# Performance work log

Hardware: AMD Instinct MI355X
Metric: run time of the kernel (lower is better)

Reference implementation:

```python
import jax, jax.numpy as jnp
import numpy as np

B, S, D, H, DH, DF, L = 8, 785, 128, 8, 64, 512, 6
HW = 28
CIN = 512


def setup_inputs() -> dict:
    key = jax.random.key(0)
    ks = iter(jax.random.split(key, 40))
    n = lambda shape, s=0.02: jax.random.normal(next(ks), shape, dtype=jnp.float32) * s
    inp = {}
    # conv stem (1x1 conv, no bias) + BN (eval mode) params
    inp["conv_w"] = n((D, CIN), 0.05)
    inp["bn_gamma"] = 1.0 + n((D,), 0.05)
    inp["bn_beta"] = n((D,), 0.05)
    inp["bn_mean"] = n((D,), 0.05)
    inp["bn_var"] = 1.0 + 0.1 * jax.random.uniform(next(ks), (D,), dtype=jnp.float32)
    # encoder embeddings
    inp["pos_emb"] = n((1, S, D))
    inp["cls_token"] = n((1, 1, D))
    # per-layer stacked params
    inp["Wq"] = n((L, D, H * DH)); inp["bq"] = jnp.zeros((L, H * DH), jnp.float32)
    inp["Wk"] = n((L, D, H * DH)); inp["bk"] = jnp.zeros((L, H * DH), jnp.float32)
    inp["Wv"] = n((L, D, H * DH)); inp["bv"] = jnp.zeros((L, H * DH), jnp.float32)
    inp["Wo"] = n((L, H * DH, D)); inp["bo"] = jnp.zeros((L, D), jnp.float32)
    inp["ln1_g"] = jnp.ones((L, D), jnp.float32); inp["ln1_b"] = jnp.zeros((L, D), jnp.float32)
    inp["ffn_w1"] = n((L, D, DF)); inp["ffn_b1"] = jnp.zeros((L, DF), jnp.float32)
    inp["ffn_w2"] = n((L, DF, D)); inp["ffn_b2"] = jnp.zeros((L, D), jnp.float32)
    inp["ln2_g"] = jnp.ones((L, D), jnp.float32); inp["ln2_b"] = jnp.zeros((L, D), jnp.float32)
    # MLP head (both Linear layers bias=False)
    inp["proj_w1"] = n((D, 512)); inp["proj_w2"] = n((512, 1))
    # forward tensor args
    inp["enc_inputs"] = jnp.ones((B, S), dtype=jnp.int32)  # no padding -> mask all False
    inp["x"] = jax.random.normal(next(ks), (B, CIN, HW, HW), dtype=jnp.float32)
    inp["y"] = jax.random.normal(next(ks), (B, CIN, HW, HW), dtype=jnp.float32)
    return inp


def _layer_norm(z, g, b, eps=1e-12):
    mu = z.mean(-1, keepdims=True)
    var = ((z - mu) ** 2).mean(-1, keepdims=True)
    return (z - mu) * jax.lax.rsqrt(var + eps) * g + b


def reference(conv_w, bn_gamma, bn_beta, bn_mean, bn_var, pos_emb, cls_token,
              Wq, bq, Wk, bk, Wv, bv, Wo, bo, ln1_g, ln1_b,
              ffn_w1, ffn_b1, ffn_w2, ffn_b2, ln2_g, ln2_b,
              proj_w1, proj_w2, enc_inputs, x, y):
    def conv_enc(z):
        z = jnp.einsum('bchw,dc->bdhw', z, conv_w)  # 1x1 conv, no bias
        inv = jax.lax.rsqrt(bn_var + 1e-5)
        z = (z - bn_mean[None, :, None, None]) * inv[None, :, None, None]
        z = z * bn_gamma[None, :, None, None] + bn_beta[None, :, None, None]
        return jax.nn.relu(z)

    x = conv_enc(x)
    y = conv_enc(y)
    max_val = jnp.maximum(x.max(), y.max())
    x = x / max_val
    y = y / max_val
    b = x.shape[0]
    x = x.reshape(b, D, -1).transpose(0, 2, 1)  # [b, hw, D]
    y = y.reshape(b, D, -1).transpose(0, 2, 1)

    cls = jnp.broadcast_to(cls_token, (b, 1, D))
    xs = jnp.concatenate([cls, x], axis=1) + pos_emb    # evolving stream (K, V)
    xf = jnp.concatenate([cls, y], axis=1) + pos_emb    # fixed stream (Q)

    pad_mask = (enc_inputs == 0)[:, None, None, :]      # [b,1,1,S], broadcast over heads & queries
    scale = 1.0 / jnp.sqrt(jnp.float32(DH))

    for i in range(L):
        q = (xf @ Wq[i] + bq[i]).reshape(b, S, H, DH).transpose(0, 2, 1, 3)
        k = (xs @ Wk[i] + bk[i]).reshape(b, S, H, DH).transpose(0, 2, 1, 3)
        v = (xs @ Wv[i] + bv[i]).reshape(b, S, H, DH).transpose(0, 2, 1, 3)
        scores = jnp.einsum('bhqd,bhkd->bhqk', q, k) * scale
        scores = jnp.where(pad_mask, jnp.float32(-1e9), scores)
        probs = jax.nn.softmax(scores, axis=-1)
        ctx = jnp.einsum('bhqk,bhkd->bhqd', probs, v)
        ctx = ctx.transpose(0, 2, 1, 3).reshape(b, S, H * DH)
        att = ctx @ Wo[i] + bo[i]
        xs = _layer_norm(xs + att, ln1_g[i], ln1_b[i])
        ff = jax.nn.gelu(xs @ ffn_w1[i] + ffn_b1[i], approximate=False) @ ffn_w2[i] + ffn_b2[i]
        xs = _layer_norm(ff + xs, ln2_g[i], ln2_b[i])

    h = jax.nn.relu(xs[:, 0, :] @ proj_w1)
    return h @ proj_w2  # [b, 1]
```

## Files before the change

### kernel.cpp

```cpp
#include <hip/hip_runtime.h>
#include <hip/hip_bf16.h>
#include <math.h>

typedef float f4 __attribute__((ext_vector_type(4)));
typedef _Float16 h8 __attribute__((ext_vector_type(8)));
typedef float f32x4 __attribute__((ext_vector_type(4)));

#define NB 8
#define NS 785
#define ND 128
#define NH 8
#define NDH 64
#define NDF 512
#define NL 6
#define NP 784
#define NCIN 512
#define NM (NB*NS)

__global__ __launch_bounds__(256) void conv_bn_relu_kernel(
    const float* __restrict__ x, const float* __restrict__ w,
    const float* __restrict__ gamma, const float* __restrict__ beta,
    const float* __restrict__ mean, const float* __restrict__ var,
    float* __restrict__ enc, unsigned int* __restrict__ maxv)
{
    __shared__ float xt[64][17];
    __shared__ float wt[64][132];
    __shared__ float red[4];
    const int b  = blockIdx.y;
    const int p0 = blockIdx.x * 16;
    const int t  = threadIdx.x;
    const int pl = (t & 3) * 4;
    const int dl = (t >> 2) * 2;
    float acc[2][4] = {};
    for (int c0 = 0; c0 < NCIN; c0 += 64) {
        __syncthreads();
        {
            int cc = t >> 2, pp = (t & 3) * 4;
            f4 v = *(const f4*)&x[(size_t)(b*NCIN + c0 + cc)*NP + p0 + pp];
            xt[cc][pp+0] = v[0]; xt[cc][pp+1] = v[1]; xt[cc][pp+2] = v[2]; xt[cc][pp+3] = v[3];
        }
        #pragma unroll
        for (int i = 0; i < 8; i++) {
            int e = t + i*256;
            int d = e >> 4, c4 = (e & 15) * 4;
            f4 v = *(const f4*)&w[(size_t)d*NCIN + c0 + c4];
            wt[c4+0][d] = v[0]; wt[c4+1][d] = v[1]; wt[c4+2][d] = v[2]; wt[c4+3][d] = v[3];
        }
        __syncthreads();
        #pragma unroll 8
        for (int cc = 0; cc < 64; cc++) {
            float w0 = wt[cc][dl], w1 = wt[cc][dl+1];
            float x0 = xt[cc][pl+0], x1 = xt[cc][pl+1], x2 = xt[cc][pl+2], x3 = xt[cc][pl+3];
            acc[0][0] += w0*x0; acc[0][1] += w0*x1; acc[0][2] += w0*x2; acc[0][3] += w0*x3;
            acc[1][0] += w1*x0; acc[1][1] += w1*x1; acc[1][2] += w1*x2; acc[1][3] += w1*x3;
        }
    }
    float lmax = 0.f;
    #pragma unroll
    for (int i = 0; i < 2; i++) {
        int d = dl + i;
        float inv = rsqrtf(var[d] + 1e-5f);
        float sc = gamma[d] * inv;
        float sh = beta[d] - mean[d] * sc;
        #pragma unroll
        for (int j = 0; j < 4; j++) {
            float vo = fmaxf(acc[i][j]*sc + sh, 0.f);
            lmax = fmaxf(lmax, vo);
            enc[(size_t)(b*NP + p0 + pl + j)*ND + d] = vo;
        }
    }
    for (int o = 1; o < 64; o <<= 1) lmax = fmaxf(lmax, __shfl_xor(lmax, o));
    if ((t & 63) == 0) red[t >> 6] = lmax;
    __syncthreads();
    if (t == 0) {
        float m2 = fmaxf(fmaxf(red[0], red[1]), fmaxf(red[2], red[3]));
        atomicMax(maxv, __float_as_uint(m2));
    }
}

__global__ __launch_bounds__(256) void wconv_kernel(
    const float* __restrict__ w0, const float* __restrict__ w1,
    const float* __restrict__ w2, const float* __restrict__ w3,
    const float* __restrict__ w4, const float* __restrict__ w5,
    _Float16* o0, _Float16* o1, _Float16* o2,
    _Float16* o3, _Float16* o4, _Float16* o5)
{
    int t = blockIdx.x*256 + threadIdx.x;
    int type = t / 393216, off = t % 393216;
    const float* in; _Float16* outp;
    switch (type) {
        case 0: in = w0; outp = o0; break;
        case 1: in = w1; outp = o1; break;
        case 2: in = w2; outp = o2; break;
        case 3: in = w3; outp = o3; break;
        case 4: in = w4; outp = o4; break;
        default: in = w5; outp = o5; break;
    }
    outp[off] = (_Float16)in[off];
}

__global__ void assemble_kernel(
    const float* __restrict__ encx, const float* __restrict__ ency,
    const float* __restrict__ cls, const float* __restrict__ pos,
    const float* __restrict__ maxv, float* __restrict__ xs,
    _Float16* __restrict__ xsh, _Float16* __restrict__ xfh)
{
    int i = blockIdx.x*256 + threadIdx.x;
    int d = i & 127;
    int s = (i >> 7) % NS;
    int b = i / (NS*ND);
    float inv = 1.f / maxv[0];
    float pv = pos[s*ND + d];
    float xv, yv;
    if (s == 0) { xv = cls[d]; yv = cls[d]; }
    else {
        int idx = (b*NP + s - 1)*ND + d;
        xv = encx[idx]*inv; yv = ency[idx]*inv;
    }
    float sx = xv + pv, fx = yv + pv;
    xs[i]  = sx;
    xsh[i] = (_Float16)sx;
    xfh[i] = (_Float16)fx;
}

template<int ACT, int OUTH>
__global__ __launch_bounds__(256) void mfma_gemm_kernel(
    const _Float16* __restrict__ A, const _Float16* __restrict__ W,
    const float* __restrict__ bias, void* __restrict__ Cv,
    int M, int N, int K)
{
    __shared__ _Float16 At[128][40];
    __shared__ _Float16 Wt[64][40];
    const int bm = blockIdx.x * 128, bn = blockIdx.y * 64;
    const int t = threadIdx.x;
    const int lane = t & 63;
    const int wave = t >> 6;
    const int m0 = (wave >> 1) * 64;
    const int n0 = (wave & 1) * 32;
    const int lrow = lane & 15, lhi = lane >> 4;
    f32x4 acc[4][2] = {};

    for (int k0 = 0; k0 < K; k0 += 32) {
        __syncthreads();
        {
            int r = t >> 1, sg = (t & 1) * 16;
            int row = bm + r;
            h8 lo = {}, hi = {};
            if (row < M) {
                const _Float16* src = &A[(size_t)row*K + k0 + sg];
                lo = *(const h8*)&src[0];
                hi = *(const h8*)&src[8];
            }
            *(h8*)&At[r][sg]     = lo;
            *(h8*)&At[r][sg + 8] = hi;
        }
        {
            int kk = t >> 3, nseg = (t & 7) * 8;
            h8 v = *(const h8*)&W[(size_t)(k0 + kk)*N + bn + nseg];
            #pragma unroll
            for (int i = 0; i < 8; i++) Wt[nseg + i][kk] = v[i];
        }
        __syncthreads();
        h8 af[4], bf[2];
        #pragma unroll
        for (int mf = 0; mf < 4; mf++) af[mf] = *(const h8*)&At[m0 + mf*16 + lrow][lhi*8];
        #pragma unroll
        for (int nf = 0; nf < 2; nf++) bf[nf] = *(const h8*)&Wt[n0 + nf*16 + lrow][lhi*8];
        #pragma unroll
        for (int mf = 0; mf < 4; mf++)
            #pragma unroll
            for (int nf = 0; nf < 2; nf++)
                acc[mf][nf] = __builtin_amdgcn_mfma_f32_16x16x32_f16(af[mf], bf[nf], acc[mf][nf], 0, 0, 0);
    }

    #pragma unroll
    for (int nf = 0; nf < 2; nf++) {
        int col = bn + n0 + nf*16 + lrow;
        float bv = bias[col];
        #pragma unroll
        for (int mf = 0; mf < 4; mf++) {
            #pragma unroll
            for (int r = 0; r < 4; r++) {
                int row = bm + m0 + mf*16 + lhi*4 + r;
                if (row < M) {
                    float v = acc[mf][nf][r] + bv;
                    if (ACT == 1) v = 0.5f * v * (1.f + erff(v * 0.70710678118654752f));
                    if (OUTH) ((_Float16*)Cv)[(size_t)row*N + col] = (_Float16)v;
                    else      ((float*)Cv)[(size_t)row*N + col] = v;
                }
            }
        }
    }
}

__global__ __launch_bounds__(256) void attn_mfma_kernel(
    const _Float16* __restrict__ Q, const _Float16* __restrict__ K,
    const _Float16* __restrict__ V, const int* __restrict__ enc,
    _Float16* __restrict__ O)
{
    __shared__ _Float16 Ks[64][68];
    __shared__ _Float16 Vt[64][68];
    __shared__ _Float16 Ps[4][16][68];
    __shared__ float madd[832];
    const int b = blockIdx.x, h = blockIdx.y, qt = blockIdx.z;
    const int q0 = qt * 64;
    const int t = threadIdx.x, lane = t & 63, w = t >> 6;
    const int lrow = lane & 15, lhi = lane >> 4;

    for (int i = t; i < 832; i += 256)
        madd[i] = (i < NS && enc[b*NS + i] == 0) ? -1e9f : 0.f;

    h8 qf[2] = {};
    {
        int qrow = q0 + w*16 + lrow;
        if (qrow < NS) {
            const _Float16* src = &Q[(size_t)(b*NS + qrow)*512 + h*64];
            #pragma unroll
            for (int ks = 0; ks < 2; ks++)
                qf[ks] = *(const h8*)&src[ks*32 + lhi*8];
        }
    }

    float m[4], l[4];
    f32x4 acc[4] = {};
    #pragma unroll
    for (int r = 0; r < 4; r++) { m[r] = -INFINITY; l[r] = 0.f; }

    for (int kt = 0; kt < 13; kt++) {
        int k0 = kt * 64;
        __syncthreads();
        {
            int r = t >> 2, c0 = (t & 3) * 16;
            int s = k0 + r;
            h8 lo = {}, hi = {};
            if (s < NS) {
                const _Float16* src = &K[(size_t)(b*NS + s)*512 + h*64 + c0];
                lo = *(const h8*)&src[0];
                hi = *(const h8*)&src[8];
            }
            *(h8*)&Ks[r][c0]     = lo;
            *(h8*)&Ks[r][c0 + 8] = hi;
        }
        {
            int r = t >> 2, c0 = (t & 3) * 16;
            int s = k0 + r;
            h8 a = {}, c = {};
            if (s < NS) {
                const _Float16* src = &V[(size_t)(b*NS + s)*512 + h*64 + c0];
                a = *(const h8*)&src[0];
                c = *(const h8*)&src[8];
            }
            #pragma unroll
            for (int i = 0; i < 8; i++) Vt[c0 + i][r] = a[i];
            #pragma unroll
            for (int i = 0; i < 8; i++) Vt[c0 + 8 + i][r] = c[i];
        }
        __syncthreads();

        f32x4 sc[4] = {};
        #pragma unroll
        for (int nf = 0; nf < 4; nf++)
            #pragma unroll
            for (int ks = 0; ks < 2; ks++) {
                h8 bf = *(const h8*)&Ks[nf*16 + lrow][ks*32 + lhi*8];
                sc[nf] = __builtin_amdgcn_mfma_f32_16x16x32_f16(qf[ks], bf, sc[nf], 0, 0, 0);
            }
        #pragma unroll
        for (int nf = 0; nf < 4; nf++) {
            int kk = k0 + nf*16 + lrow;
            float ma = madd[kk];
            bool oob = (kk >= NS);
            #pragma unroll
            for (int r = 0; r < 4; r++) {
                float v = sc[nf][r] * 0.125f + ma;
                sc[nf][r] = oob ? -INFINITY : v;
            }
        }
        float corr[4];
        #pragma unroll
        for (int r = 0; r < 4; r++) {
            float mt = fmaxf(fmaxf(sc[0][r], sc[1][r]), fmaxf(sc[2][r], sc[3][r]));
            mt = fmaxf(mt, __shfl_xor(mt, 1));
            mt = fmaxf(mt, __shfl_xor(mt, 2));
            mt = fmaxf(mt, __shfl_xor(mt, 4));
            mt = fmaxf(mt, __shfl_xor(mt, 8));
            float mn = fmaxf(m[r], mt);
            corr[r] = __expf(m[r] - mn);
            m[r] = mn;
            float ps = 0.f;
            #pragma unroll
            for (int nf = 0; nf < 4; nf++) {
                float p = __expf(sc[nf][r] - mn);
                sc[nf][r] = p;
                ps += p;
            }
            ps += __shfl_xor(ps, 1);
            ps += __shfl_xor(ps, 2);
            ps += __shfl_xor(ps, 4);
            ps += __shfl_xor(ps, 8);
            l[r] = l[r] * corr[r] + ps;
        }
        #pragma unroll
        for (int nf = 0; nf < 4; nf++)
            #pragma unroll
            for (int r = 0; r < 4; r++)
                Ps[w][lhi*4 + r][nf*16 + lrow] = (_Float16)sc[nf][r];
        asm volatile("s_waitcnt lgkmcnt(0)" ::: "memory");
        __builtin_amdgcn_sched_barrier(0);
        #pragma unroll
        for (int nf = 0; nf < 4; nf++)
            #pragma unroll
            for (int r = 0; r < 4; r++) acc[nf][r] *= corr[r];
        #pragma unroll
        for (int nf = 0; nf < 4; nf++)
            #pragma unroll
            for (int ks = 0; ks < 2; ks++) {
                h8 pf = *(const h8*)&Ps[w][lrow][ks*32 + lhi*8];
                h8 vf = *(const h8*)&Vt[nf*16 + lrow][ks*32 + lhi*8];
                acc[nf] = __builtin_amdgcn_mfma_f32_16x16x32_f16(pf, vf, acc[nf], 0, 0, 0);
            }
    }
    #pragma unroll
    for (int nf = 0; nf < 4; nf++)
        #pragma unroll
        for (int r = 0; r < 4; r++) {
            int row = q0 + w*16 + lhi*4 + r;
            if (row < NS)
                O[(size_t)(b*NS + row)*512 + h*64 + nf*16 + lrow] = (_Float16)(acc[nf][r] / l[r]);
        }
}

__global__ __launch_bounds__(256) void res_ln_kernel(
    const float* X, const float* __restrict__ R,
    const float* __restrict__ g, const float* __restrict__ be,
    float* out, _Float16* __restrict__ outh)
{
    int row = blockIdx.x*4 + (threadIdx.x >> 6);
    int lane = threadIdx.x & 63;
    const float* xr = X + (size_t)row*128;
    const float* rr = R + (size_t)row*128;
    float a0 = xr[lane] + rr[lane];
    float a1 = xr[lane+64] + rr[lane+64];
    float s = a0 + a1;
    for (int o = 1; o < 64; o <<= 1) s += __shfl_xor(s, o);
    float mean = s * (1.f/128.f);
    float e0 = a0 - mean, e1 = a1 - mean;
    float vs = e0*e0 + e1*e1;
    for (int o = 1; o < 64; o <<= 1) vs += __shfl_xor(vs, o);
    float rstd = rsqrtf(vs * (1.f/128.f) + 1e-12f);
    float o0 = e0*rstd*g[lane] + be[lane];
    float o1 = e1*rstd*g[lane+64] + be[lane+64];
    out[(size_t)row*128 + lane]       = o0;
    out[(size_t)row*128 + lane + 64]  = o1;
    outh[(size_t)row*128 + lane]      = (_Float16)o0;
    outh[(size_t)row*128 + lane + 64] = (_Float16)o1;
}

__global__ __launch_bounds__(512) void head_kernel(
    const float* __restrict__ xs, const float* __restrict__ w1,
    const float* __restrict__ w2, float* __restrict__ out)
{
    __shared__ float red[8];
    int b = blockIdx.x, j = threadIdx.x;
    const float* xr = xs + (size_t)(b*NS)*128;
    float acc = 0.f;
    #pragma unroll 8
    for (int c = 0; c < 128; c++) acc += xr[c] * w1[c*512 + j];
    acc = fmaxf(acc, 0.f);
    float sv = acc * w2[j];
    for (int o = 1; o < 64; o <<= 1) sv += __shfl_xor(sv, o);
    if ((j & 63) == 0) red[j >> 6] = sv;
    __syncthreads();
    if (j == 0) {
        float r = 0.f;
        #pragma unroll
        for (int i = 0; i < 8; i++) r += red[i];
        out[b] = r;
    }
}

extern "C" void kernel_launch(void* const* d_in, const int* in_sizes, int n_in,
                              void* d_out, int out_size, void* d_ws, size_t ws_size,
                              hipStream_t stream)
{
    const float* conv_w   = (const float*)d_in[0];
    const float* bn_gamma = (const float*)d_in[1];
    const float* bn_beta  = (const float*)d_in[2];
    const float* bn_mean  = (const float*)d_in[3];
    const float* bn_var   = (const float*)d_in[4];
    const float* pos_emb  = (const float*)d_in[5];
    const float* cls_tok  = (const float*)d_in[6];
    const float* Wq = (const float*)d_in[7];  const float* bq = (const float*)d_in[8];
    const float* Wk = (const float*)d_in[9];  const float* bk = (const float*)d_in[10];
    const float* Wv = (const float*)d_in[11]; const float* bv = (const float*)d_in[12];
    const float* Wo = (const float*)d_in[13]; const float* bo = (const float*)d_in[14];
    const float* ln1_g = (const float*)d_in[15]; const float* ln1_b = (const float*)d_in[16];
    const float* fw1 = (const float*)d_in[17]; const float* fb1 = (const float*)d_in[18];
    const float* fw2 = (const float*)d_in[19]; const float* fb2 = (const float*)d_in[20];
    const float* ln2_g = (const float*)d_in[21]; const float* ln2_b = (const float*)d_in[22];
    const float* pw1 = (const float*)d_in[23]; const float* pw2 = (const float*)d_in[24];
    const int*   enc = (const int*)d_in[25];
    const float* x   = (const float*)d_in[26];
    const float* y   = (const float*)d_in[27];
    float* out = (float*)d_out;

    char* base = (char*)d_ws;
    size_t o = 0;
    auto alloc = [&](size_t bytes) { void* p = base + o; o += bytes; return p; };
    float* maxv     = (float*)alloc(256);
    float* xs       = (float*)alloc(3215360);
    float* fout     = (float*)alloc(3215360);
    float* encx     = (float*)alloc(3211264);
    float* ency     = (float*)alloc(3211264);
    _Float16* xsh   = (_Float16*)alloc(1607680);
    _Float16* xfh   = (_Float16*)alloc(1607680);
    _Float16* qh    = (_Float16*)alloc(6430720);
    _Float16* kh    = (_Float16*)alloc(6430720);
    _Float16* vh    = (_Float16*)alloc(6430720);
    _Float16* ctxh  = (_Float16*)alloc(6430720);
    _Float16* fmidh = (_Float16*)alloc(6430720);
    _Float16* wqh   = (_Float16*)alloc(786432);
    _Float16* wkh   = (_Float16*)alloc(786432);
    _Float16* wvh   = (_Float16*)alloc(786432);
    _Float16* woh   = (_Float16*)alloc(786432);
    _Float16* f1h   = (_Float16*)alloc(786432);
    _Float16* f2h   = (_Float16*)alloc(786432);

    hipMemsetAsync(d_ws, 0, 256, stream);

    wconv_kernel<<<9216, 256, 0, stream>>>(Wq, Wk, Wv, Wo, fw1, fw2,
                                           wqh, wkh, wvh, woh, f1h, f2h);

    dim3 cgrid(49, NB);
    conv_bn_relu_kernel<<<cgrid, 256, 0, stream>>>(x, conv_w, bn_gamma, bn_beta,
        bn_mean, bn_var, encx, (unsigned int*)maxv);
    conv_bn_relu_kernel<<<cgrid, 256, 0, stream>>>(y, conv_w, bn_gamma, bn_beta,
        bn_mean, bn_var, ency, (unsigned int*)maxv);

    assemble_kernel<<<3140, 256, 0, stream>>>(encx, ency, cls_tok, pos_emb, maxv,
                                              xs, xsh, xfh);

    for (int i = 0; i < NL; i++) {
        const size_t wofs = (size_t)i * 128 * 512;
        mfma_gemm_kernel<0,1><<<dim3(50,8), 256, 0, stream>>>(xfh, wqh + wofs, bq + i*512, qh, NM, 512, 128);
        mfma_gemm_kernel<0,1><<<dim3(50,8), 256, 0, stream>>>(xsh, wkh + wofs, bk + i*512, kh, NM, 512, 128);
        mfma_gemm_kernel<0,1><<<dim3(50,8), 256, 0, stream>>>(xsh, wvh + wofs, bv + i*512, vh, NM, 512, 128);
        attn_mfma_kernel<<<dim3(8,8,13), 256, 0, stream>>>(qh, kh, vh, enc, ctxh);
        mfma_gemm_kernel<0,0><<<dim3(50,2), 256, 0, stream>>>(ctxh, woh + wofs, bo + i*128, fout, NM, 128, 512);
        res_ln_kernel<<<1570, 256, 0, stream>>>(xs, fout, ln1_g + i*128, ln1_b + i*128, xs, xsh);
        mfma_gemm_kernel<1,1><<<dim3(50,8), 256, 0, stream>>>(xsh, f1h + wofs, fb1 + i*512, fmidh, NM, 512, 128);
        mfma_gemm_kernel<0,0><<<dim3(50,2), 256, 0, stream>>>(fmidh, f2h + wofs, fb2 + i*128, fout, NM, 128, 512);
        res_ln_kernel<<<1570, 256, 0, stream>>>(xs, fout, ln2_g + i*128, ln2_b + i*128, xs, xsh);
    }

    head_kernel<<<8, 512, 0, stream>>>(xs, pw1, pw2, out);
}
```

Measured before the change: 1.142 ms.

## Split attention over key range into two partial passes plus combine kernel

Each attention block now processes only half of the key tiles, doubling the grid, and writes unnormalized fp16 partial outputs plus per-row max and sum statistics. A new combine kernel merges the two partials with log-sum-exp rescaling into the context buffer. The aim is more parallelism and shorter per-block latency in attention. In exchange it adds an extra kernel launch, extra global memory traffic for the partial outputs, and fp16 storage of unnormalized accumulators.

```diff
diff --git a/kernel.cpp b/kernel.cpp
--- a/kernel.cpp
+++ b/kernel.cpp
@@ -196,14 +196,18 @@
 __global__ __launch_bounds__(256) void attn_mfma_kernel(
     const _Float16* __restrict__ Q, const _Float16* __restrict__ K,
     const _Float16* __restrict__ V, const int* __restrict__ enc,
-    _Float16* __restrict__ O)
+    _Float16* __restrict__ Op0, _Float16* __restrict__ Op1,
+    float* __restrict__ mlbuf)
 {
     __shared__ _Float16 Ks[64][68];
     __shared__ _Float16 Vt[64][68];
     __shared__ _Float16 Ps[4][16][68];
     __shared__ float madd[832];
-    const int b = blockIdx.x, h = blockIdx.y, qt = blockIdx.z;
+    const int b = blockIdx.x, h = blockIdx.y;
+    const int qt = blockIdx.z >> 1, split = blockIdx.z & 1;
     const int q0 = qt * 64;
+    const int ktbeg = split ? 7 : 0, ktend = split ? 13 : 7;
+    _Float16* Op = split ? Op1 : Op0;
     const int t = threadIdx.x, lane = t & 63, w = t >> 6;
     const int lrow = lane & 15, lhi = lane >> 4;
 
@@ -226,7 +230,7 @@
     #pragma unroll
     for (int r = 0; r < 4; r++) { m[r] = -INFINITY; l[r] = 0.f; }
 
-    for (int kt = 0; kt < 13; kt++) {
+    for (int kt = ktbeg; kt < ktend; kt++) {
         int k0 = kt * 64;
         __syncthreads();
         {
@@ -326,8 +330,38 @@
         for (int r = 0; r < 4; r++) {
             int row = q0 + w*16 + lhi*4 + r;
             if (row < NS)
-                O[(size_t)(b*NS + row)*512 + h*64 + nf*16 + lrow] = (_Float16)(acc[nf][r] / l[r]);
-        }
+                Op[(size_t)(b*NS + row)*512 + h*64 + nf*16 + lrow] = (_Float16)acc[nf][r];
+        }
+    if (lrow == 0) {
+        #pragma unroll
+        for (int r = 0; r < 4; r++) {
+            int row = q0 + w*16 + lhi*4 + r;
+            if (row < NS) {
+                size_t idx = (size_t)(((split*NB + b)*NH + h)*NS + row) * 2;
+                mlbuf[idx]     = m[r];
+                mlbuf[idx + 1] = l[r];
+            }
+        }
+    }
+}
+
+__global__ __launch_bounds__(256) void attn_combine_kernel(
+    const _Float16* __restrict__ Op0, const _Float16* __restrict__ Op1,
+    const float* __restrict__ mlbuf, _Float16* __restrict__ O)
+{
+    int i = blockIdx.x*256 + threadIdx.x;
+    int d = i & 511;
+    int row = (i >> 9) % NS;
+    int b = i / (NS*512);
+    int h = d >> 6;
+    size_t i0 = (size_t)(((0*NB + b)*NH + h)*NS + row) * 2;
+    size_t i1 = (size_t)(((1*NB + b)*NH + h)*NS + row) * 2;
+    float m0 = mlbuf[i0], l0 = mlbuf[i0+1];
+    float m1 = mlbuf[i1], l1 = mlbuf[i1+1];
+    float mm = fmaxf(m0, m1);
+    float w0 = __expf(m0 - mm), w1 = __expf(m1 - mm);
+    float o0 = (float)Op0[i], o1 = (float)Op1[i];
+    O[i] = (_Float16)((o0*w0 + o1*w1) / (l0*w0 + l1*w1));
 }
 
 __global__ __launch_bounds__(256) void res_ln_kernel(
@@ -419,6 +453,9 @@
     _Float16* vh    = (_Float16*)alloc(6430720);
     _Float16* ctxh  = (_Float16*)alloc(6430720);
     _Float16* fmidh = (_Float16*)alloc(6430720);
+    _Float16* op0   = (_Float16*)alloc(6430720);
+    _Float16* op1   = (_Float16*)alloc(6430720);
+    float* mlbuf    = (float*)alloc(803840);
     _Float16* wqh   = (_Float16*)alloc(786432);
     _Float16* wkh   = (_Float16*)alloc(786432);
     _Float16* wvh   = (_Float16*)alloc(786432);
@@ -445,7 +482,8 @@
         mfma_gemm_kernel<0,1><<<dim3(50,8), 256, 0, stream>>>(xfh, wqh + wofs, bq + i*512, qh, NM, 512, 128);
         mfma_gemm_kernel<0,1><<<dim3(50,8), 256, 0, stream>>>(xsh, wkh + wofs, bk + i*512, kh, NM, 512, 128);
         mfma_gemm_kernel<0,1><<<dim3(50,8), 256, 0, stream>>>(xsh, wvh + wofs, bv + i*512, vh, NM, 512, 128);
-        attn_mfma_kernel<<<dim3(8,8,13), 256, 0, stream>>>(qh, kh, vh, enc, ctxh);
+        attn_mfma_kernel<<<dim3(8,8,26), 256, 0, stream>>>(qh, kh, vh, enc, op0, op1, mlbuf);
+        attn_combine_kernel<<<12560, 256, 0, stream>>>(op0, op1, mlbuf, ctxh);
         mfma_gemm_kernel<0,0><<<dim3(50,2), 256, 0, stream>>>(ctxh, woh + wofs, bo + i*128, fout, NM, 128, 512);
         res_ln_kernel<<<1570, 256, 0, stream>>>(xs, fout, ln1_g + i*128, ln1_b + i*128, xs, xsh);
         mfma_gemm_kernel<1,1><<<dim3(50,8), 256, 0, stream>>>(xsh, f1h + wofs, fb1 + i*512, fmidh, NM, 512, 128);
```

Result: no change. 1.132 ms (-0.9%).
